# Kernel optimization log

Hardware: AMD Instinct MI355X
Metric: run time of the kernel (lower is better)

The kernel has to match this reference:

```python
import jax, jax.numpy as jnp
import numpy as np

EPS = 1e-8  # torch F.cosine_similarity eps


def setup_inputs() -> dict:
    key = jax.random.key(0)
    k1, k2 = jax.random.split(key)
    B, D = 8192, 512
    return {
        "label_tensor": jnp.arange(B, dtype=jnp.int64),
        "feature_a": jax.random.normal(k1, (B, D), dtype=jnp.float32),
        "feature_b": jax.random.normal(k2, (B, D), dtype=jnp.float32),
        "affine_w": jnp.ones((1,), dtype=jnp.float32),   # AffineModel scale
        "affine_b": jnp.zeros((1,), dtype=jnp.float32),  # AffineModel bias
    }


def reference(label_tensor, feature_a, feature_b, affine_w, affine_b):
    # cos_score[i, j] = cos(a_i, b_j): normalize then one [B,D]x[D,B] GEMM
    a_n = feature_a / jnp.maximum(
        jnp.linalg.norm(feature_a, axis=1, keepdims=True), EPS)
    b_n = feature_b / jnp.maximum(
        jnp.linalg.norm(feature_b, axis=1, keepdims=True), EPS)
    cos_score = jnp.einsum("id,jd->ij", a_n, b_n)  # [B, B]
    cos_score = affine_w[0] * cos_score + affine_b[0]  # AffineModel
    # cross-entropy with labels = arange(B) -> diagonal of log_softmax
    logp = jax.nn.log_softmax(cos_score, axis=1)
    B = cos_score.shape[0]
    loss = -jnp.mean(logp[jnp.arange(B), jnp.arange(B)])
    return (loss, cos_score)
```

## Files before the change

### kernel.cpp

```cpp
#include <hip/hip_runtime.h>
#include <hip/hip_bf16.h>

#define B_ROWS 8192
#define DIM 512

typedef __bf16 bf16x8 __attribute__((ext_vector_type(8)));
typedef float f32x4 __attribute__((ext_vector_type(4)));

__device__ inline ushort f2bf(float x) {
    __hip_bfloat16 h = __float2bfloat16(x);
    return __builtin_bit_cast(ushort, h);
}

__global__ __launch_bounds__(256) void norm_kernel(const float* __restrict__ A,
                                                   const float* __restrict__ Bf,
                                                   ushort* __restrict__ An,
                                                   ushort* __restrict__ Bn) {
    int gw = (blockIdx.x * 256 + threadIdx.x) >> 6;
    int lane = threadIdx.x & 63;
    const float* src;
    ushort* dst;
    if (gw < B_ROWS) {
        src = A + (size_t)gw * DIM;
        dst = An + (size_t)gw * DIM;
    } else {
        src = Bf + (size_t)(gw - B_ROWS) * DIM;
        dst = Bn + (size_t)(gw - B_ROWS) * DIM;
    }
    const float4* s4 = (const float4*)src;
    float4 v0 = s4[lane * 2];
    float4 v1 = s4[lane * 2 + 1];
    float ss = v0.x * v0.x + v0.y * v0.y + v0.z * v0.z + v0.w * v0.w
             + v1.x * v1.x + v1.y * v1.y + v1.z * v1.z + v1.w * v1.w;
#pragma unroll
    for (int m = 32; m >= 1; m >>= 1) ss += __shfl_xor(ss, m, 64);
    float scale = 1.0f / fmaxf(sqrtf(ss), 1e-8f);
    union { ushort us[8]; uint4 q; } o;
    o.us[0] = f2bf(v0.x * scale); o.us[1] = f2bf(v0.y * scale);
    o.us[2] = f2bf(v0.z * scale); o.us[3] = f2bf(v0.w * scale);
    o.us[4] = f2bf(v1.x * scale); o.us[5] = f2bf(v1.y * scale);
    o.us[6] = f2bf(v1.z * scale); o.us[7] = f2bf(v1.w * scale);
    ((uint4*)dst)[lane] = o.q;
}

#define GLDS(src, dst) __builtin_amdgcn_global_load_lds( \
    (const __attribute__((address_space(1))) unsigned int*)(src), \
    (__attribute__((address_space(3))) unsigned int*)(dst), 16, 0, 0)

#define STG(bufv, ab, PTR, doff, ktv) do {                                   \
    GLDS((PTR) + (ktv) * 64,      L + (((bufv)*2 + (ab))*2 + 0)*8192 + (doff)); \
    GLDS((PTR) + (ktv) * 64 + 32, L + (((bufv)*2 + (ab))*2 + 1)*8192 + (doff)); } while (0)

#define BARRIER() asm volatile("s_barrier" ::: "memory")

__global__ __launch_bounds__(512, 2) void gemm_kernel(
    const ushort* __restrict__ An, const ushort* __restrict__ Bn,
    float* __restrict__ C, float* __restrict__ rowpart,
    const float* __restrict__ wp, const float* __restrict__ bp) {
    __shared__ ushort lds[2][2][2][8192];
    ushort* L = &lds[0][0][0][0];

    const int t = threadIdx.x;
    const int brow = blockIdx.y * 256;
    const int bcol = blockIdx.x * 256;
    const int wid = t >> 6, lane = t & 63;
    const int wr = wid >> 2, wc = wid & 3;
    const int fr = lane & 15;
    const int fhi = lane >> 4;

    const int schunk8 = ((t & 3) ^ ((t >> 3) & 3)) * 8;
    const int srowAa = (t >> 8) * 128 + ((t >> 2) & 63);
    const int srowBa = (t >> 7) * 64 + ((t >> 2) & 31);
    const ushort* pAa = An + (size_t)(brow + srowAa) * DIM + schunk8;
    const ushort* pAb = An + (size_t)(brow + srowAa + 64) * DIM + schunk8;
    const ushort* pBa = Bn + (size_t)(bcol + srowBa) * DIM + schunk8;
    const ushort* pBb = Bn + (size_t)(bcol + srowBa + 32) * DIM + schunk8;
    const int dAa = t * 8 + (t >> 8) * 2048;
    const int dAb = dAa + 2048;
    const int dBa = t * 8 + (t >> 7) * 1024;
    const int dBb = dBa + 1024;

    const int rchunk8 = (fhi ^ ((fr >> 1) & 3)) * 8;

    f32x4 acc[8][4];
#pragma unroll
    for (int i = 0; i < 8; i++)
#pragma unroll
        for (int j = 0; j < 4; j++) acc[i][j] = (f32x4){0.f, 0.f, 0.f, 0.f};

    bf16x8 af[4][2], b0[2][2], b1[2][2];

    auto rdA = [&](int buf, int mb) {
#pragma unroll
        for (int i = 0; i < 4; ++i)
#pragma unroll
            for (int kk = 0; kk < 2; ++kk)
                af[i][kk] = *(const bf16x8*)(L + ((buf * 2 + 0) * 2 + kk) * 8192
                            + (wr * 128 + (mb + i) * 16 + fr) * 32 + rchunk8);
    };
    auto rdB = [&](bf16x8 (&b)[2][2], int buf, int nb) {
#pragma unroll
        for (int j = 0; j < 2; ++j)
#pragma unroll
            for (int kk = 0; kk < 2; ++kk)
                b[j][kk] = *(const bf16x8*)(L + ((buf * 2 + 1) * 2 + kk) * 8192
                           + (wc * 64 + (nb + j) * 16 + fr) * 32 + rchunk8);
    };
    auto mfma16 = [&](bf16x8 (&b)[2][2], int mb, int nb) {
        __builtin_amdgcn_sched_barrier(0);
        __builtin_amdgcn_s_setprio(1);
#pragma unroll
        for (int i = 0; i < 4; ++i)
#pragma unroll
            for (int j = 0; j < 2; ++j)
#pragma unroll
                for (int kk = 0; kk < 2; ++kk)
                    acc[mb + i][nb + j] = __builtin_amdgcn_mfma_f32_16x16x32_bf16(
                        af[i][kk], b[j][kk], acc[mb + i][nb + j], 0, 0, 0);
        __builtin_amdgcn_s_setprio(0);
        __builtin_amdgcn_sched_barrier(0);
    };

    STG(0, 0, pAa, dAa, 0);
    STG(0, 1, pBa, dBa, 0);
    STG(0, 0, pAb, dAb, 0);
    STG(0, 1, pBb, dBb, 0);
    asm volatile("s_waitcnt vmcnt(0)\n\ts_barrier" ::: "memory");

#pragma unroll
    for (int kt = 0; kt < 8; ++kt) {
        const int cur = kt & 1, nxt = cur ^ 1;
        if (kt < 7) STG(nxt, 0, pAa, dAa, kt + 1);
        rdA(cur, 0);
        rdB(b0, cur, 0);
        BARRIER();
        mfma16(b0, 0, 0);
        if (kt == 7) { asm volatile("s_waitcnt vmcnt(0)\n\ts_barrier" ::: "memory"); }
        else         { asm volatile("s_waitcnt vmcnt(2)\n\ts_barrier" ::: "memory"); }
        if (kt < 7) STG(nxt, 1, pBa, dBa, kt + 1);
        rdB(b1, cur, 2);
        BARRIER();
        mfma16(b1, 0, 2);
        BARRIER();
        if (kt < 7) STG(nxt, 0, pAb, dAb, kt + 1);
        rdA(cur, 4);
        BARRIER();
        mfma16(b1, 4, 2);
        BARRIER();
        if (kt < 7) STG(nxt, 1, pBb, dBb, kt + 1);
        BARRIER();
        mfma16(b0, 4, 0);
        if (kt < 7) { asm volatile("s_waitcnt vmcnt(4)\n\ts_barrier" ::: "memory"); }
        else        { BARRIER(); }
    }

    __syncthreads();
    const float w = wp[0], bb = bp[0];
    const float M = fabsf(w) + fabsf(bb);
    float* part = (float*)L;
#pragma unroll
    for (int m = 0; m < 8; ++m) {
#pragma unroll
        for (int r = 0; r < 4; ++r) {
            const int rloc = wr * 128 + m * 16 + fhi * 4 + r;
            const size_t grow = (size_t)(brow + rloc);
            float psum = 0.f;
#pragma unroll
            for (int n = 0; n < 4; ++n) {
                const int gcol = bcol + wc * 64 + n * 16 + fr;
                float s = fmaf(w, acc[m][n][r], bb);
                C[grow * B_ROWS + gcol] = s;
                psum += __expf(s - M);
            }
#pragma unroll
            for (int msk = 1; msk <= 8; msk <<= 1) psum += __shfl_xor(psum, msk, 64);
            if (fr == 0) part[wc * 256 + rloc] = psum;
        }
    }
    __syncthreads();
    if (t < 256) {
        float s = part[t] + part[256 + t] + part[512 + t] + part[768 + t];
        rowpart[(size_t)blockIdx.x * B_ROWS + brow + t] = s;
    }
}

__global__ __launch_bounds__(256) void loss_kernel(const float* __restrict__ C,
                                                   const float* __restrict__ rowpart,
                                                   const float* __restrict__ wp,
                                                   const float* __restrict__ bp,
                                                   float* __restrict__ out0) {
    __shared__ float sred[4];
    const int row = blockIdx.x * 256 + threadIdx.x;
    float rs = 0.f;
#pragma unroll
    for (int j = 0; j < 32; ++j) rs += rowpart[(size_t)j * B_ROWS + row];
    const float M = fabsf(wp[0]) + fabsf(bp[0]);
    const float sii = C[(size_t)row * B_ROWS + row];
    float v = sii - M - __logf(rs);
#pragma unroll
    for (int msk = 32; msk >= 1; msk >>= 1) v += __shfl_xor(v, msk, 64);
    if ((threadIdx.x & 63) == 0) sred[threadIdx.x >> 6] = v;
    __syncthreads();
    if (threadIdx.x == 0) {
        float tot = sred[0] + sred[1] + sred[2] + sred[3];
        atomicAdd(out0, -tot / (float)B_ROWS);
    }
}

extern "C" void kernel_launch(void* const* d_in, const int* in_sizes, int n_in,
                              void* d_out, int out_size, void* d_ws, size_t ws_size,
                              hipStream_t stream) {
    const float* A  = (const float*)d_in[1];
    const float* Bf = (const float*)d_in[2];
    const float* wp = (const float*)d_in[3];
    const float* bp = (const float*)d_in[4];
    float* out = (float*)d_out;

    ushort* An = (ushort*)d_ws;
    ushort* Bn = An + (size_t)B_ROWS * DIM;
    float* rowpart = (float*)((char*)d_ws + (size_t)2 * B_ROWS * DIM * sizeof(ushort));

    hipMemsetAsync(d_out, 0, sizeof(float), stream);
    norm_kernel<<<dim3(16384 * 64 / 256), 256, 0, stream>>>(A, Bf, An, Bn);
    dim3 grid(B_ROWS / 256, B_ROWS / 256);
    gemm_kernel<<<grid, 512, 0, stream>>>(An, Bn, out + 1, rowpart, wp, bp);
    loss_kernel<<<B_ROWS / 256, 256, 0, stream>>>(out + 1, rowpart, wp, bp, out);
}
```

Measured before the change: 387.7 us.

## Stage GEMM epilogue through LDS for coalesced stores and remap block order

The epilogue now writes the accumulator tile into swizzled LDS in two phases and then writes out full 16-byte vectors per thread along each row. This replaces the scattered 4-byte stores of the 256MB score matrix, and the row exp-sums are now computed from the staged rows with a 4-lane shuffle. The grid becomes 1D with a block-index remap that spreads consecutive blocks across the 8 XCDs so each XCD works on a contiguous band of tiles, aiming for better L2 reuse. The cost is two extra barriers and the LDS round trip in the epilogue.

```diff
diff --git a/kernel.cpp b/kernel.cpp
--- a/kernel.cpp
+++ b/kernel.cpp
@@ -61,8 +61,11 @@
     ushort* L = &lds[0][0][0][0];
 
     const int t = threadIdx.x;
-    const int brow = blockIdx.y * 256;
-    const int bcol = blockIdx.x * 256;
+    const int bid = blockIdx.x;
+    const int orig = ((bid & 7) << 7) | (bid >> 3);
+    const int by = orig >> 5, bx = orig & 31;
+    const int brow = by * 256;
+    const int bcol = bx * 256;
     const int wid = t >> 6, lane = t & 63;
     const int wr = wid >> 2, wc = wid & 3;
     const int fr = lane & 15;
@@ -157,30 +160,48 @@
     __syncthreads();
     const float w = wp[0], bb = bp[0];
     const float M = fabsf(w) + fabsf(bb);
-    float* part = (float*)L;
-#pragma unroll
-    for (int m = 0; m < 8; ++m) {
-#pragma unroll
-        for (int r = 0; r < 4; ++r) {
-            const int rloc = wr * 128 + m * 16 + fhi * 4 + r;
-            const size_t grow = (size_t)(brow + rloc);
-            float psum = 0.f;
-#pragma unroll
-            for (int n = 0; n < 4; ++n) {
-                const int gcol = bcol + wc * 64 + n * 16 + fr;
-                float s = fmaf(w, acc[m][n][r], bb);
-                C[grow * B_ROWS + gcol] = s;
-                psum += __expf(s - M);
+    float* FL = (float*)L;
+
+    const int rrow = t >> 2;
+    const int rx = (rrow >> 2) & 3;
+    const int xr = rx ^ (rrow & 1);
+    const int rc0 = t & 3;
+    const int rwr = rrow >> 6, rwithin = rrow & 63;
+
+#pragma unroll
+    for (int ph = 0; ph < 2; ++ph) {
+#pragma unroll
+        for (int mm = 0; mm < 4; ++mm) {
+            const int m = 4 * ph + mm;
+#pragma unroll
+            for (int r = 0; r < 4; ++r) {
+                const int wrow = wr * 64 + mm * 16 + fhi * 4 + r;
+                const int xw = (fhi ^ (r & 1)) << 4;
+#pragma unroll
+                for (int n = 0; n < 4; ++n) {
+                    const int col = (wc * 64 + n * 16 + fr) ^ xw;
+                    FL[wrow * 256 + col] = fmaf(w, acc[m][n][r], bb);
+                }
             }
-#pragma unroll
-            for (int msk = 1; msk <= 8; msk <<= 1) psum += __shfl_xor(psum, msk, 64);
-            if (fr == 0) part[wc * 256 + rloc] = psum;
         }
-    }
-    __syncthreads();
-    if (t < 256) {
-        float s = part[t] + part[256 + t] + part[512 + t] + part[768 + t];
-        rowpart[(size_t)blockIdx.x * B_ROWS + brow + t] = s;
+        __syncthreads();
+        const int rowfull = rwr * 128 + 64 * ph + rwithin;
+        const size_t grow = (size_t)(brow + rowfull);
+        float* crow = C + grow * B_ROWS + bcol;
+        float psum = 0.f;
+#pragma unroll
+        for (int i = 0; i < 16; ++i) {
+            const int c4 = rc0 + 4 * i;
+            const int c4s = c4 ^ (xr << 2);
+            f32x4 v = *(const f32x4*)&FL[rrow * 256 + c4s * 4];
+            *(f32x4*)(crow + 4 * c4) = v;
+            psum += __expf(v[0] - M) + __expf(v[1] - M)
+                  + __expf(v[2] - M) + __expf(v[3] - M);
+        }
+        psum += __shfl_xor(psum, 1, 64);
+        psum += __shfl_xor(psum, 2, 64);
+        if (rc0 == 0) rowpart[(size_t)bx * B_ROWS + grow] = psum;
+        __syncthreads();
     }
 }
 
@@ -222,7 +243,6 @@
 
     hipMemsetAsync(d_out, 0, sizeof(float), stream);
     norm_kernel<<<dim3(16384 * 64 / 256), 256, 0, stream>>>(A, Bf, An, Bn);
-    dim3 grid(B_ROWS / 256, B_ROWS / 256);
-    gemm_kernel<<<grid, 512, 0, stream>>>(An, Bn, out + 1, rowpart, wp, bp);
+    gemm_kernel<<<dim3(1024), 512, 0, stream>>>(An, Bn, out + 1, rowpart, wp, bp);
     loss_kernel<<<B_ROWS / 256, 256, 0, stream>>>(out + 1, rowpart, wp, bp, out);
 }
```

New measurement: 391.3 us. No clear change (+0.9%).
